# Optimization experiments

Hardware: AMD Instinct MI355X
Metric: run time of the kernel (lower is better)

## Reference

```python
import jax, jax.numpy as jnp
import numpy as np

NX, DX, H, DO = 8192, 8, 1024, 1


def setup_inputs() -> dict:
    key = jax.random.key(0)
    ks = jax.random.split(key, 7)
    s1 = 1.0 / np.sqrt(DX)  # torch Linear default init bound
    s2 = 1.0 / np.sqrt(H)
    x = jax.random.normal(ks[0], (NX, DX), jnp.float32)
    W1 = jax.random.uniform(ks[1], (H, DX), jnp.float32, -s1, s1)
    b1 = jax.random.uniform(ks[2], (H,), jnp.float32, -s1, s1)
    W2 = jax.random.uniform(ks[3], (H, H), jnp.float32, -s2, s2)
    b2 = jax.random.uniform(ks[4], (H,), jnp.float32, -s2, s2)
    W3 = jax.random.uniform(ks[5], (DO, H), jnp.float32, -s2, s2)
    b3 = jax.random.uniform(ks[6], (DO,), jnp.float32, -s2, s2)
    return {"x": x, "W1": W1, "b1": b1, "W2": W2, "b2": b2, "W3": W3, "b3": b3}


def reference(x, W1, b1, W2, b2, W3, b3):
    # Forward: Linear -> Tanh -> Linear -> Tanh -> Linear
    z1 = jnp.tanh(x @ W1.T + b1)          # [nx, h]
    z2 = jnp.tanh(z1 @ W2.T + b2)         # [nx, h]
    y = z2 @ W3.T + b3                    # [nx, out]

    # DerivTanh(h) = 4/(e^-h + e^h)^2 = sech^2(h) = 1 - tanh(h)^2
    d1 = 1.0 - z1 * z1                    # [nx, h]
    d2 = 1.0 - z2 * z2                    # [nx, h]

    # Vectorized analytic Jacobian (original loops over each input dim k):
    # tmp_k = d2 * (W2 @ (d1 * W1[:, k]))  then  dydx_k = W3 @ tmp_k
    J = d1[:, :, None] * W1[None, :, :]                    # [nx, h, dx]
    J = d2[:, :, None] * jnp.einsum('ij,njk->nik', W2, J)  # [nx, h, dx]
    dydx = jnp.einsum('oj,njk->nok', W3, J)                # [nx, out, dx]
    # Match original list-of-dx ordering: dydx[k] has shape [nx, out]
    dydx = jnp.transpose(dydx, (2, 0, 1))                  # [dx, nx, out]
    return y, dydx
```

## Files before the change

### kernel.cpp

```cpp
#include <hip/hip_runtime.h>
#include <stdint.h>

#define NXS 8192
#define HS  1024

typedef __attribute__((ext_vector_type(8))) short short8;
typedef __attribute__((ext_vector_type(4))) float f32x4;

__device__ __forceinline__ float bf2f(uint32_t b) {
    union { uint32_t u; float f; } c; c.u = b << 16; return c.f;
}
__device__ __forceinline__ uint16_t f2bf(float f) {
    union { float f; uint32_t u; } c; c.f = f;
    return (uint16_t)((c.u + 0x7fffu + ((c.u >> 16) & 1u)) >> 16);
}
__device__ __forceinline__ void async_cp16(const void* g, void* l) {
    __builtin_amdgcn_global_load_lds(
        (const __attribute__((address_space(1))) void*)g,
        (__attribute__((address_space(3))) void*)l,
        16, 0, 0);
}

__global__ __launch_bounds__(256) void k01(
    const float* __restrict__ x, const float* __restrict__ W1,
    const float* __restrict__ b1, const float* __restrict__ W2,
    const float* __restrict__ b3, uint16_t* __restrict__ Z1,
    uint16_t* __restrict__ W2c, uint16_t* __restrict__ W2T,
    float* __restrict__ out)
{
    __shared__ uint16_t tile[64][65];
    const int b = blockIdx.x;
    if (b < 8192) {
        const int n = b;
        const int j = threadIdx.x * 4;
        float4 x0 = *(const float4*)(x + n * 8);
        float4 x1 = *(const float4*)(x + n * 8 + 4);
        float4 bb = *(const float4*)(b1 + j);
        float sv[4] = {bb.x, bb.y, bb.z, bb.w};
        ushort4 o;
        uint16_t* op = (uint16_t*)&o;
#pragma unroll
        for (int c = 0; c < 4; ++c) {
            float4 w0 = *(const float4*)(W1 + (j + c) * 8);
            float4 w1 = *(const float4*)(W1 + (j + c) * 8 + 4);
            float s = sv[c]
                + x0.x * w0.x + x0.y * w0.y + x0.z * w0.z + x0.w * w0.w
                + x1.x * w1.x + x1.y * w1.y + x1.z * w1.z + x1.w * w1.w;
            op[c] = f2bf(tanhf(s));
        }
        *(ushort4*)(Z1 + (size_t)n * HS + j) = o;
    } else if (b < 8448) {
        const int bb2 = b - 8192;
        const int bx = bb2 & 15, by = bb2 >> 4;
        const int tx = threadIdx.x & 63, ty = threadIdx.x >> 6;
#pragma unroll
        for (int rr = 0; rr < 64; rr += 4) {
            int r = ty + rr;
            uint16_t v = f2bf(W2[(size_t)(by * 64 + r) * HS + bx * 64 + tx]);
            W2c[(size_t)(by * 64 + r) * HS + bx * 64 + tx] = v;
            tile[r][tx] = v;
        }
        __syncthreads();
#pragma unroll
        for (int rr = 0; rr < 64; rr += 4)
            W2T[(size_t)(bx * 64 + ty + rr) * HS + by * 64 + tx] = tile[tx][ty + rr];
    } else {
        const int idx = (b - 8448) * 256 + threadIdx.x;
        out[idx] = (idx < NXS) ? b3[0] : 0.f;
    }
}

template <int MODE>
__global__ __launch_bounds__(512, 4) void gemm_k(
    const uint16_t* __restrict__ A, const uint16_t* __restrict__ B,
    const float* __restrict__ bias, const float* __restrict__ W3,
    uint16_t* __restrict__ Out, float* __restrict__ yOut,
    const uint16_t* __restrict__ Z1, const float* __restrict__ W1,
    float* __restrict__ dOut)
{
    __shared__ __attribute__((aligned(16))) uint16_t smem[32768];
    const int t = threadIdx.x;
    const int wave = t >> 6, lane = t & 63;
    const int lq = lane >> 4, lr = lane & 15;
    const int wm = wave >> 1, wn = wave & 1;
    const int rowBase = blockIdx.x * 128;
    const int colBase = blockIdx.y * 128;

    const int s0 = t, s1 = 512 + t;
    const int r0 = s0 >> 3, q0 = (s0 & 7) ^ (r0 & 7);
    const int r1 = s1 >> 3, q1 = (s1 & 7) ^ (r1 & 7);
    const uint16_t* gA0 = A + (size_t)(rowBase + r0) * HS + q0 * 8;
    const uint16_t* gA1 = A + (size_t)(rowBase + r1) * HS + q1 * 8;
    const uint16_t* gB0 = B + (size_t)(colBase + r0) * HS + q0 * 8;
    const uint16_t* gB1 = B + (size_t)(colBase + r1) * HS + q1 * 8;

    f32x4 acc[2][4] = {};

    async_cp16(gA0, (char*)smem + s0 * 16);
    async_cp16(gA1, (char*)smem + s1 * 16);
    async_cp16(gB0, (char*)smem + 32768 + s0 * 16);
    async_cp16(gB1, (char*)smem + 32768 + s1 * 16);
    __syncthreads();

    int buf = 0;
    for (int k0 = 0; k0 < HS; k0 += 64, buf ^= 1) {
        if (k0 + 64 < HS) {
            const int ko = k0 + 64;
            const int bo = (buf ^ 1) * 16384;
            async_cp16(gA0 + ko, (char*)smem + bo + s0 * 16);
            async_cp16(gA1 + ko, (char*)smem + bo + s1 * 16);
            async_cp16(gB0 + ko, (char*)smem + 32768 + bo + s0 * 16);
            async_cp16(gB1 + ko, (char*)smem + 32768 + bo + s1 * 16);
        }
        const short* pA = (const short*)smem + buf * 8192;
        const short* pB = (const short*)smem + 16384 + buf * 8192;
#pragma unroll
        for (int kk = 0; kk < 64; kk += 32) {
            const int kq = (kk >> 3) + lq;
            short8 af[2], bfr[4];
#pragma unroll
            for (int ti = 0; ti < 2; ++ti) {
                int ar = wm * 32 + ti * 16 + lr;
                af[ti] = *(const short8*)(pA + ar * 64 + ((kq ^ (ar & 7)) << 3));
            }
#pragma unroll
            for (int tj = 0; tj < 4; ++tj) {
                int br = wn * 64 + tj * 16 + lr;
                bfr[tj] = *(const short8*)(pB + br * 64 + ((kq ^ (br & 7)) << 3));
            }
#pragma unroll
            for (int ti = 0; ti < 2; ++ti)
#pragma unroll
                for (int tj = 0; tj < 4; ++tj)
                    acc[ti][tj] = __builtin_amdgcn_mfma_f32_16x16x32_bf16(
                        af[ti], bfr[tj], acc[ti][tj], 0, 0, 0);
        }
        __syncthreads();
    }

    if (MODE == 0) {
        float cB[4], cW[4]; int cCol[4];
#pragma unroll
        for (int tj = 0; tj < 4; ++tj) {
            cCol[tj] = colBase + wn * 64 + tj * 16 + lr;
            cB[tj] = bias[cCol[tj]];
            cW[tj] = W3[cCol[tj]];
        }
#pragma unroll
        for (int ti = 0; ti < 2; ++ti) {
#pragma unroll
            for (int r = 0; r < 4; ++r) {
                int row = rowBase + wm * 32 + ti * 16 + lq * 4 + r;
                float ys = 0.f;
#pragma unroll
                for (int tj = 0; tj < 4; ++tj) {
                    float z2 = tanhf(acc[ti][tj][r] + cB[tj]);
                    ys += z2 * cW[tj];
                    Out[(size_t)row * HS + cCol[tj]] = f2bf((1.f - z2 * z2) * cW[tj]);
                }
                ys += __shfl_xor(ys, 1); ys += __shfl_xor(ys, 2);
                ys += __shfl_xor(ys, 4); ys += __shfl_xor(ys, 8);
                if (lr == 0) atomicAdd(&yOut[row], ys);
            }
        }
    } else {
#pragma unroll
        for (int ti = 0; ti < 2; ++ti)
#pragma unroll
            for (int r = 0; r < 4; ++r) {
                int rowl = wm * 32 + ti * 16 + lq * 4 + r;
                const size_t zrow = (size_t)(rowBase + rowl) * HS + colBase;
#pragma unroll
                for (int tj = 0; tj < 4; ++tj) {
                    int coll = wn * 64 + tj * 16 + lr;
                    float z1 = bf2f(Z1[zrow + coll]);
                    smem[rowl * 136 + coll] =
                        f2bf(acc[ti][tj][r] * (1.f - z1 * z1));
                }
            }
        __syncthreads();
        short8 w1f[4];
#pragma unroll
        for (int kb = 0; kb < 4; ++kb) {
            short8 v;
#pragma unroll
            for (int j = 0; j < 8; ++j) {
                float w = (lr < 8)
                    ? W1[(size_t)(colBase + kb * 32 + lq * 8 + j) * 8 + lr] : 0.f;
                ((short*)&v)[j] = (short)f2bf(w);
            }
            w1f[kb] = v;
        }
        f32x4 dd = {};
#pragma unroll
        for (int kb = 0; kb < 4; ++kb) {
            short8 aF = *(const short8*)(smem + (wave * 16 + lr) * 136
                                         + kb * 32 + lq * 8);
            dd = __builtin_amdgcn_mfma_f32_16x16x32_bf16(aF, w1f[kb], dd, 0, 0, 0);
        }
        if (lr < 8) {
            int row = rowBase + wave * 16 + lq * 4;
#pragma unroll
            for (int rg = 0; rg < 4; ++rg)
                atomicAdd(&dOut[(size_t)lr * NXS + row + rg], dd[rg]);
        }
    }
}

extern "C" void kernel_launch(void* const* d_in, const int* in_sizes, int n_in,
                              void* d_out, int out_size, void* d_ws, size_t ws_size,
                              hipStream_t stream) {
    (void)in_sizes; (void)n_in; (void)out_size; (void)ws_size;
    const float* x  = (const float*)d_in[0];
    const float* W1 = (const float*)d_in[1];
    const float* b1 = (const float*)d_in[2];
    const float* W2 = (const float*)d_in[3];
    const float* b2 = (const float*)d_in[4];
    const float* W3 = (const float*)d_in[5];
    const float* b3 = (const float*)d_in[6];
    float* out = (float*)d_out;

    char* ws = (char*)d_ws;
    uint16_t* Z1  = (uint16_t*)(ws);
    uint16_t* V   = (uint16_t*)(ws + (size_t)16 * 1024 * 1024);
    uint16_t* W2c = (uint16_t*)(ws + (size_t)32 * 1024 * 1024);
    uint16_t* W2T = (uint16_t*)(ws + (size_t)34 * 1024 * 1024);

    k01<<<8736, 256, 0, stream>>>(x, W1, b1, W2, b3, Z1, W2c, W2T, out);
    gemm_k<0><<<dim3(NXS / 128, HS / 128), 512, 0, stream>>>(
        Z1, W2c, b2, W3, V, out, nullptr, nullptr, nullptr);
    gemm_k<1><<<dim3(NXS / 128, HS / 128), 512, 0, stream>>>(
        V, W2T, nullptr, nullptr, nullptr, nullptr, Z1, W1, out + NXS);
}
```

Before: 151.6 us.

## Shrink GEMM tiles, batch layer-1 rows per block, pretranspose W1 to bf16

```diff
diff --git a/kernel.cpp b/kernel.cpp
--- a/kernel.cpp
+++ b/kernel.cpp
@@ -26,33 +26,44 @@
     const float* __restrict__ b1, const float* __restrict__ W2,
     const float* __restrict__ b3, uint16_t* __restrict__ Z1,
     uint16_t* __restrict__ W2c, uint16_t* __restrict__ W2T,
-    float* __restrict__ out)
+    uint16_t* __restrict__ W1T, float* __restrict__ out)
 {
+    __shared__ float xs[8][8];
     __shared__ uint16_t tile[64][65];
     const int b = blockIdx.x;
-    if (b < 8192) {
-        const int n = b;
-        const int j = threadIdx.x * 4;
-        float4 x0 = *(const float4*)(x + n * 8);
-        float4 x1 = *(const float4*)(x + n * 8 + 4);
-        float4 bb = *(const float4*)(b1 + j);
-        float sv[4] = {bb.x, bb.y, bb.z, bb.w};
-        ushort4 o;
-        uint16_t* op = (uint16_t*)&o;
+    const int t = threadIdx.x;
+    if (b < 1024) {
+        const int n0 = b * 8;
+        if (t < 64) xs[t >> 3][t & 7] = x[n0 * 8 + t];
+        const int j = t * 4;
+        float w[4][8];
 #pragma unroll
         for (int c = 0; c < 4; ++c) {
             float4 w0 = *(const float4*)(W1 + (j + c) * 8);
             float4 w1 = *(const float4*)(W1 + (j + c) * 8 + 4);
-            float s = sv[c]
-                + x0.x * w0.x + x0.y * w0.y + x0.z * w0.z + x0.w * w0.w
-                + x1.x * w1.x + x1.y * w1.y + x1.z * w1.z + x1.w * w1.w;
-            op[c] = f2bf(tanhf(s));
-        }
-        *(ushort4*)(Z1 + (size_t)n * HS + j) = o;
-    } else if (b < 8448) {
-        const int bb2 = b - 8192;
+            w[c][0] = w0.x; w[c][1] = w0.y; w[c][2] = w0.z; w[c][3] = w0.w;
+            w[c][4] = w1.x; w[c][5] = w1.y; w[c][6] = w1.z; w[c][7] = w1.w;
+        }
+        float4 bb = *(const float4*)(b1 + j);
+        const float bv[4] = {bb.x, bb.y, bb.z, bb.w};
+        __syncthreads();
+#pragma unroll
+        for (int s = 0; s < 8; ++s) {
+            ushort4 o;
+            uint16_t* op = (uint16_t*)&o;
+#pragma unroll
+            for (int c = 0; c < 4; ++c) {
+                float sum = bv[c];
+#pragma unroll
+                for (int k = 0; k < 8; ++k) sum += xs[s][k] * w[c][k];
+                op[c] = f2bf(tanhf(sum));
+            }
+            *(ushort4*)(Z1 + (size_t)(n0 + s) * HS + j) = o;
+        }
+    } else if (b < 1280) {
+        const int bb2 = b - 1024;
         const int bx = bb2 & 15, by = bb2 >> 4;
-        const int tx = threadIdx.x & 63, ty = threadIdx.x >> 6;
+        const int tx = t & 63, ty = t >> 6;
 #pragma unroll
         for (int rr = 0; rr < 64; rr += 4) {
             int r = ty + rr;
@@ -64,77 +75,74 @@
 #pragma unroll
         for (int rr = 0; rr < 64; rr += 4)
             W2T[(size_t)(bx * 64 + ty + rr) * HS + by * 64 + tx] = tile[tx][ty + rr];
+    } else if (b < 1568) {
+        const int idx = (b - 1280) * 256 + t;
+        out[idx] = (idx < NXS) ? b3[0] : 0.f;
     } else {
-        const int idx = (b - 8448) * 256 + threadIdx.x;
-        out[idx] = (idx < NXS) ? b3[0] : 0.f;
+        const int idx = (b - 1568) * 256 + t;
+        const int r = idx >> 10, c = idx & 1023;
+        W1T[idx] = (r < 8) ? f2bf(W1[c * 8 + r]) : (uint16_t)0;
     }
 }
 
 template <int MODE>
-__global__ __launch_bounds__(512, 4) void gemm_k(
+__global__ __launch_bounds__(256, 4) void gemm_k(
     const uint16_t* __restrict__ A, const uint16_t* __restrict__ B,
     const float* __restrict__ bias, const float* __restrict__ W3,
     uint16_t* __restrict__ Out, float* __restrict__ yOut,
-    const uint16_t* __restrict__ Z1, const float* __restrict__ W1,
+    const uint16_t* __restrict__ Z1, const uint16_t* __restrict__ W1T,
     float* __restrict__ dOut)
 {
-    __shared__ __attribute__((aligned(16))) uint16_t smem[32768];
+    __shared__ __attribute__((aligned(16))) uint16_t smem[12288];
     const int t = threadIdx.x;
     const int wave = t >> 6, lane = t & 63;
     const int lq = lane >> 4, lr = lane & 15;
     const int wm = wave >> 1, wn = wave & 1;
-    const int rowBase = blockIdx.x * 128;
+    const int rowBase = blockIdx.x * 64;
     const int colBase = blockIdx.y * 128;
 
-    const int s0 = t, s1 = 512 + t;
-    const int r0 = s0 >> 3, q0 = (s0 & 7) ^ (r0 & 7);
-    const int r1 = s1 >> 3, q1 = (s1 & 7) ^ (r1 & 7);
-    const uint16_t* gA0 = A + (size_t)(rowBase + r0) * HS + q0 * 8;
-    const uint16_t* gA1 = A + (size_t)(rowBase + r1) * HS + q1 * 8;
-    const uint16_t* gB0 = B + (size_t)(colBase + r0) * HS + q0 * 8;
-    const uint16_t* gB1 = B + (size_t)(colBase + r1) * HS + q1 * 8;
+    const int rA = t >> 2, qA = (t & 3) ^ (rA & 3);
+    const int sB0 = t, sB1 = 256 + t;
+    const int rB0 = sB0 >> 2, qB0 = (sB0 & 3) ^ (rB0 & 3);
+    const int rB1 = sB1 >> 2, qB1 = (sB1 & 3) ^ (rB1 & 3);
+    const uint16_t* gA  = A + (size_t)(rowBase + rA) * HS + qA * 8;
+    const uint16_t* gB0 = B + (size_t)(colBase + rB0) * HS + qB0 * 8;
+    const uint16_t* gB1 = B + (size_t)(colBase + rB1) * HS + qB1 * 8;
 
     f32x4 acc[2][4] = {};
 
-    async_cp16(gA0, (char*)smem + s0 * 16);
-    async_cp16(gA1, (char*)smem + s1 * 16);
-    async_cp16(gB0, (char*)smem + 32768 + s0 * 16);
-    async_cp16(gB1, (char*)smem + 32768 + s1 * 16);
+    async_cp16(gA,  (char*)smem + t * 16);
+    async_cp16(gB0, (char*)smem + 8192 + sB0 * 16);
+    async_cp16(gB1, (char*)smem + 8192 + sB1 * 16);
     __syncthreads();
 
     int buf = 0;
-    for (int k0 = 0; k0 < HS; k0 += 64, buf ^= 1) {
-        if (k0 + 64 < HS) {
-            const int ko = k0 + 64;
-            const int bo = (buf ^ 1) * 16384;
-            async_cp16(gA0 + ko, (char*)smem + bo + s0 * 16);
-            async_cp16(gA1 + ko, (char*)smem + bo + s1 * 16);
-            async_cp16(gB0 + ko, (char*)smem + 32768 + bo + s0 * 16);
-            async_cp16(gB1 + ko, (char*)smem + 32768 + bo + s1 * 16);
-        }
-        const short* pA = (const short*)smem + buf * 8192;
-        const short* pB = (const short*)smem + 16384 + buf * 8192;
-#pragma unroll
-        for (int kk = 0; kk < 64; kk += 32) {
-            const int kq = (kk >> 3) + lq;
-            short8 af[2], bfr[4];
-#pragma unroll
-            for (int ti = 0; ti < 2; ++ti) {
-                int ar = wm * 32 + ti * 16 + lr;
-                af[ti] = *(const short8*)(pA + ar * 64 + ((kq ^ (ar & 7)) << 3));
-            }
-#pragma unroll
-            for (int tj = 0; tj < 4; ++tj) {
-                int br = wn * 64 + tj * 16 + lr;
-                bfr[tj] = *(const short8*)(pB + br * 64 + ((kq ^ (br & 7)) << 3));
-            }
-#pragma unroll
-            for (int ti = 0; ti < 2; ++ti)
-#pragma unroll
-                for (int tj = 0; tj < 4; ++tj)
-                    acc[ti][tj] = __builtin_amdgcn_mfma_f32_16x16x32_bf16(
-                        af[ti], bfr[tj], acc[ti][tj], 0, 0, 0);
-        }
+    for (int k0 = 0; k0 < HS; k0 += 32, buf ^= 1) {
+        if (k0 + 32 < HS) {
+            const int ko = k0 + 32;
+            async_cp16(gA + ko,  (char*)smem + (buf ^ 1) * 4096 + t * 16);
+            async_cp16(gB0 + ko, (char*)smem + 8192 + (buf ^ 1) * 8192 + sB0 * 16);
+            async_cp16(gB1 + ko, (char*)smem + 8192 + (buf ^ 1) * 8192 + sB1 * 16);
+        }
+        const short* pA = (const short*)smem + buf * 2048;
+        const short* pB = (const short*)smem + 4096 + buf * 4096;
+        short8 af[2], bfr[4];
+#pragma unroll
+        for (int ti = 0; ti < 2; ++ti) {
+            int ar = wm * 32 + ti * 16 + lr;
+            af[ti] = *(const short8*)(pA + ar * 32 + ((lq ^ (ar & 3)) << 3));
+        }
+#pragma unroll
+        for (int tj = 0; tj < 4; ++tj) {
+            int br = wn * 64 + tj * 16 + lr;
+            bfr[tj] = *(const short8*)(pB + br * 32 + ((lq ^ (br & 3)) << 3));
+        }
+#pragma unroll
+        for (int ti = 0; ti < 2; ++ti)
+#pragma unroll
+            for (int tj = 0; tj < 4; ++tj)
+                acc[ti][tj] = __builtin_amdgcn_mfma_f32_16x16x32_bf16(
+                    af[ti], bfr[tj], acc[ti][tj], 0, 0, 0);
         __syncthreads();
     }
 
@@ -179,24 +187,14 @@
                 }
             }
         __syncthreads();
-        short8 w1f[4];
-#pragma unroll
-        for (int kb = 0; kb < 4; ++kb) {
-            short8 v;
-#pragma unroll
-            for (int j = 0; j < 8; ++j) {
-                float w = (lr < 8)
-                    ? W1[(size_t)(colBase + kb * 32 + lq * 8 + j) * 8 + lr] : 0.f;
-                ((short*)&v)[j] = (short)f2bf(w);
-            }
-            w1f[kb] = v;
-        }
         f32x4 dd = {};
 #pragma unroll
         for (int kb = 0; kb < 4; ++kb) {
             short8 aF = *(const short8*)(smem + (wave * 16 + lr) * 136
                                          + kb * 32 + lq * 8);
-            dd = __builtin_amdgcn_mfma_f32_16x16x32_bf16(aF, w1f[kb], dd, 0, 0, 0);
+            short8 bF = *(const short8*)(W1T + lr * HS + colBase
+                                         + kb * 32 + lq * 8);
+            dd = __builtin_amdgcn_mfma_f32_16x16x32_bf16(aF, bF, dd, 0, 0, 0);
         }
         if (lr < 8) {
             int row = rowBase + wave * 16 + lq * 4;
@@ -225,10 +223,11 @@
     uint16_t* V   = (uint16_t*)(ws + (size_t)16 * 1024 * 1024);
     uint16_t* W2c = (uint16_t*)(ws + (size_t)32 * 1024 * 1024);
     uint16_t* W2T = (uint16_t*)(ws + (size_t)34 * 1024 * 1024);
-
-    k01<<<8736, 256, 0, stream>>>(x, W1, b1, W2, b3, Z1, W2c, W2T, out);
-    gemm_k<0><<<dim3(NXS / 128, HS / 128), 512, 0, stream>>>(
+    uint16_t* W1T = (uint16_t*)(ws + (size_t)36 * 1024 * 1024);
+
+    k01<<<1632, 256, 0, stream>>>(x, W1, b1, W2, b3, Z1, W2c, W2T, W1T, out);
+    gemm_k<0><<<dim3(NXS / 64, HS / 128), 256, 0, stream>>>(
         Z1, W2c, b2, W3, V, out, nullptr, nullptr, nullptr);
-    gemm_k<1><<<dim3(NXS / 128, HS / 128), 512, 0, stream>>>(
-        V, W2T, nullptr, nullptr, nullptr, nullptr, Z1, W1, out + NXS);
-}
+    gemm_k<1><<<dim3(NXS / 64, HS / 128), 256, 0, stream>>>(
+        V, W2T, nullptr, nullptr, nullptr, nullptr, Z1, W1T, out + NXS);
+}
```

New measurement: 147.2 us. 2.9% less time.
